# Kernel optimization log

Measured on AMD Instinct MI355X. Metric: run time of the kernel, lower is better.

## Reference

```python
import jax, jax.numpy as jnp
import numpy as np

DIM = 256
NUM_HEADS = 8
WH, WW = 7, 7
N = WH * WW
HEAD_DIM = DIM // NUM_HEADS
SCALE = HEAD_DIM ** -0.5
B_ = 4096
NW = 64  # windows per image


def _relative_position_index():
    # Swin relative position index: (N, N) int32 in [0, (2Wh-1)*(2Ww-1))
    coords = np.stack(np.meshgrid(np.arange(WH), np.arange(WW), indexing='ij'))  # (2, Wh, Ww)
    cf = coords.reshape(2, -1)  # (2, N)
    rel = cf[:, :, None] - cf[:, None, :]  # (2, N, N)
    rel = rel.transpose(1, 2, 0).copy()
    rel[:, :, 0] += WH - 1
    rel[:, :, 1] += WW - 1
    rel[:, :, 0] *= 2 * WW - 1
    return jnp.asarray(rel.sum(-1), dtype=jnp.int32)  # (N, N)


def setup_inputs() -> dict:
    key = jax.random.key(0)
    ks = jax.random.split(key, 7)
    x = jax.random.normal(ks[0], (B_, N, DIM), dtype=jnp.float32)
    mask = jax.random.normal(ks[1], (NW, N, N), dtype=jnp.float32)
    qkv_w = jax.random.normal(ks[2], (3 * DIM, DIM), dtype=jnp.float32) * 0.02
    qkv_b = jnp.zeros((3 * DIM,), dtype=jnp.float32)
    proj_w = jax.random.normal(ks[3], (DIM, DIM), dtype=jnp.float32) * 0.02
    proj_b = jnp.zeros((DIM,), dtype=jnp.float32)
    bias_table = jax.random.normal(ks[4], ((2 * WH - 1) * (2 * WW - 1), NUM_HEADS), dtype=jnp.float32) * 0.02
    rel_index = _relative_position_index()
    return {"x": x, "mask": mask, "qkv_w": qkv_w, "qkv_b": qkv_b,
            "proj_w": proj_w, "proj_b": proj_b, "bias_table": bias_table,
            "rel_index": rel_index}


def reference(x, mask, qkv_w, qkv_b, proj_w, proj_b, bias_table, rel_index):
    Bw, n, c = x.shape
    # qkv projection: (B_, N, 3C) -> (3, B_, nH, N, hd)
    qkv = (x @ qkv_w.T + qkv_b).reshape(Bw, n, 3, NUM_HEADS, HEAD_DIM)
    qkv = qkv.transpose(2, 0, 3, 1, 4)
    q, k, v = qkv[0], qkv[1], qkv[2]
    attn = jnp.einsum('bhqd,bhkd->bhqk', q * SCALE, k)  # (B_, nH, N, N)
    # gathered relative position bias: (nH, N, N)
    rpb = bias_table[rel_index.reshape(-1)].reshape(n, n, NUM_HEADS).transpose(2, 0, 1)
    attn = attn + rpb[None]
    # window mask: reshape batch into (B, nW) and broadcast mask per-window
    nW = mask.shape[0]
    attn = attn.reshape(Bw // nW, nW, NUM_HEADS, n, n) + mask[None, :, None]
    attn = attn.reshape(Bw, NUM_HEADS, n, n)
    attn = jax.nn.softmax(attn, axis=-1)
    out = jnp.einsum('bhqk,bhkd->bhqd', attn, v)  # (B_, nH, N, hd)
    out = out.transpose(0, 2, 1, 3).reshape(Bw, n, c)
    return out @ proj_w.T + proj_b
```

## Files before the change

### kernel.cpp

```cpp
#include <hip/hip_runtime.h>
#include <hip/hip_bf16.h>

typedef __bf16 bf16;
typedef __bf16 bf16x8 __attribute__((ext_vector_type(8)));
typedef float  f32x4  __attribute__((ext_vector_type(4)));

#define MFMA16(A,B,C) __builtin_amdgcn_mfma_f32_16x16x32_bf16((A),(B),(C),0,0,0)

constexpr float SCALE = 0.17677669529663687f;

constexpr size_t CB_OFF    = 0;
constexpr size_t QKVW_OFF  = 8388608;
constexpr size_t PROJW_OFF = QKVW_OFF + 768*256*2;
constexpr size_t QI_OFF    = PROJW_OFF + 256*256*2;
constexpr size_t TEN_ELEMS = 51380224ull;
constexpr size_t AO_OFF    = QI_OFF + 3*TEN_ELEMS*2;

__global__ __launch_bounds__(256) void build_cb_kernel(
    const float* __restrict__ bias_table, const float* __restrict__ mask,
    const int* __restrict__ rel_index, float* __restrict__ cb) {
  int idx = blockIdx.x * 256 + threadIdx.x;
  int j = idx & 63, m = (idx >> 6) & 63, h = (idx >> 12) & 7, w = idx >> 15;
  float v = 0.f;
  if (j < 49 && m < 49)
    v = bias_table[rel_index[m * 49 + j] * 8 + h] + mask[(w * 49 + m) * 49 + j];
  cb[idx] = v;
}

__global__ __launch_bounds__(256) void cvt_w_kernel(
    const float* __restrict__ qkv_w, const float* __restrict__ proj_w,
    bf16* __restrict__ qkv_wb, bf16* __restrict__ proj_wb) {
  int i = blockIdx.x * 256 + threadIdx.x;
  if (i < 768 * 256) qkv_wb[i] = (bf16)qkv_w[i];
  else               proj_wb[i - 768 * 256] = (bf16)proj_w[i - 768 * 256];
}

__device__ __forceinline__ bf16x8 frag(const bf16* S, int row, int kchunk) {
  return *reinterpret_cast<const bf16x8*>(&S[row * 64 + ((kchunk ^ (row & 7)) * 8)]);
}

__global__ __launch_bounds__(512, 2) void gemm_qkv_kernel(
    const float* __restrict__ x, const bf16* __restrict__ qkv_wb,
    const float* __restrict__ qkv_b, bf16* __restrict__ qkv_i) {
  __shared__ __align__(16) bf16 As[128 * 64];
  __shared__ __align__(16) bf16 Bs[256 * 64];
  const int bid = blockIdx.x;
  const int xcd = bid & 7, idx = bid >> 3;
  const int m_t = xcd * 196 + idx / 3;
  const int n_t = idx % 3;
  const int tid = threadIdx.x;
  const int wv = tid >> 6, l = tid & 63, l15 = l & 15, lgp = l >> 4;
  const int wr = wv >> 2, wc = wv & 3;

  const f32x4 fzero = {0.f, 0.f, 0.f, 0.f};
  f32x4 acc[4][4];
#pragma unroll
  for (int mt = 0; mt < 4; ++mt)
#pragma unroll
    for (int nt = 0; nt < 4; ++nt) acc[mt][nt] = fzero;

  for (int ks = 0; ks < 4; ++ks) {
    const int k0 = ks * 64;
#pragma unroll
    for (int i = 0; i < 2; ++i) {
      int c = i * 512 + tid;
      int row = c >> 3, kc = c & 7;
      const float* src = x + (size_t)(m_t * 128 + row) * 256 + k0 + kc * 8;
      f32x4 f0 = *reinterpret_cast<const f32x4*>(src);
      f32x4 f1 = *reinterpret_cast<const f32x4*>(src + 4);
      bf16x8 v8;
#pragma unroll
      for (int e = 0; e < 4; ++e) { v8[e] = (bf16)f0[e]; v8[e + 4] = (bf16)f1[e]; }
      *reinterpret_cast<bf16x8*>(&As[row * 64 + ((kc ^ (row & 7)) * 8)]) = v8;
    }
#pragma unroll
    for (int i = 0; i < 4; ++i) {
      int c = i * 512 + tid;
      int row = c >> 3, kc = c & 7;
      bf16x8 w8 = *reinterpret_cast<const bf16x8*>(
          qkv_wb + (size_t)(n_t * 256 + row) * 256 + k0 + kc * 8);
      *reinterpret_cast<bf16x8*>(&Bs[row * 64 + ((kc ^ (row & 7)) * 8)]) = w8;
    }
    __syncthreads();
#pragma unroll
    for (int kk = 0; kk < 2; ++kk) {
      bf16x8 Af[4], Bf[4];
#pragma unroll
      for (int mt = 0; mt < 4; ++mt) Af[mt] = frag(As, wr * 64 + mt * 16 + l15, kk * 4 + lgp);
#pragma unroll
      for (int nt = 0; nt < 4; ++nt) Bf[nt] = frag(Bs, wc * 64 + nt * 16 + l15, kk * 4 + lgp);
#pragma unroll
      for (int mt = 0; mt < 4; ++mt)
#pragma unroll
        for (int nt = 0; nt < 4; ++nt) acc[mt][nt] = MFMA16(Af[mt], Bf[nt], acc[mt][nt]);
    }
    __syncthreads();
  }

  bf16* tb = qkv_i + (size_t)n_t * TEN_ELEMS;
  const float sc = (n_t == 0) ? SCALE : 1.0f;
  float bias[4]; int hh[4], dd[4];
#pragma unroll
  for (int nt = 0; nt < 4; ++nt) {
    int n_g = n_t * 256 + wc * 64 + nt * 16 + l15;
    bias[nt] = qkv_b[n_g];
    int nl = n_g & 255;
    hh[nt] = nl >> 5; dd[nt] = nl & 31;
  }
#pragma unroll
  for (int mt = 0; mt < 4; ++mt) {
#pragma unroll
    for (int r = 0; r < 4; ++r) {
      int r_g = m_t * 128 + wr * 64 + mt * 16 + lgp * 4 + r;
      int b = r_g / 49, m = r_g - b * 49;
#pragma unroll
      for (int nt = 0; nt < 4; ++nt) {
        tb[((size_t)(b * 8 + hh[nt]) * 49 + m) * 32 + dd[nt]] =
            (bf16)((acc[mt][nt][r] + bias[nt]) * sc);
      }
    }
  }
}

__device__ __forceinline__ bf16x8 repack8(f32x4 Ta, f32x4 Tb, int l15, int lgp) {
  const int s0 = l15 + ((lgp & 1) << 5);
  const bool hi = (lgp & 2) != 0;
  bf16x8 F;
#pragma unroll
  for (int r = 0; r < 4; ++r) {
    float a0 = __shfl(Ta[r], s0);
    float b0 = __shfl(Tb[r], s0);
    F[r] = (bf16)(hi ? b0 : a0);
    float a1 = __shfl(Ta[r], s0 + 16);
    float b1 = __shfl(Tb[r], s0 + 16);
    F[r + 4] = (bf16)(hi ? b1 : a1);
  }
  return F;
}

__global__ __launch_bounds__(256) void attn_kernel(
    const bf16* __restrict__ qkv_i, const float* __restrict__ cb,
    bf16* __restrict__ ao) {
  __shared__ __align__(16) bf16 Vs[4][64 * 32];
  const int tid = threadIdx.x, wv = tid >> 6, l = tid & 63;
  const int l15 = l & 15, lgp = l >> 4;
  const int g = blockIdx.x * 4 + wv;
  const int b = g >> 3, h = g & 7;

  const bf16* qp = qkv_i + (size_t)(b * 8 + h) * 1568;
  const bf16* kp = qp + TEN_ELEMS;
  const bf16* vp = kp + TEN_ELEMS;
  bf16* vsm = &Vs[wv][0];

#pragma unroll
  for (int i = 0; i < 4; ++i) {
    int c = i * 64 + l;
    if (c < 196)
      *reinterpret_cast<bf16x8*>(&vsm[c * 8]) =
          *reinterpret_cast<const bf16x8*>(vp + c * 8);
  }
  {
    const bf16x8 z8 = {(bf16)0.f,(bf16)0.f,(bf16)0.f,(bf16)0.f,
                       (bf16)0.f,(bf16)0.f,(bf16)0.f,(bf16)0.f};
    if (l < 60) *reinterpret_cast<bf16x8*>(&vsm[1568 + l * 8]) = z8;
  }
  __syncthreads();

  bf16x8 Qf[4], Kf[4];
#pragma unroll
  for (int mt = 0; mt < 4; ++mt) {
    int m = mt * 16 + l15; int mc = m < 49 ? m : 48;
    Qf[mt] = *reinterpret_cast<const bf16x8*>(qp + mc * 32 + lgp * 8);
  }
#pragma unroll
  for (int jt = 0; jt < 4; ++jt) {
    int j = jt * 16 + l15; int jc = j < 49 ? j : 48;
    Kf[jt] = *reinterpret_cast<const bf16x8*>(kp + jc * 32 + lgp * 8);
  }
  bf16x8 Vb[2][2];
#pragma unroll
  for (int dt = 0; dt < 2; ++dt)
#pragma unroll
    for (int ksx = 0; ksx < 2; ++ksx) {
#pragma unroll
      for (int u = 0; u < 8; ++u) {
        int j = ksx * 32 + lgp * 8 + u;
        Vb[dt][ksx][u] = vsm[j * 32 + dt * 16 + l15];
      }
    }

  const float* cbp = cb + (size_t)((b & 63) * 8 + h) * 4096;
  bf16* aob = ao + (size_t)b * 12544;
  const f32x4 fzero = {0.f, 0.f, 0.f, 0.f};

#pragma unroll
  for (int mt = 0; mt < 4; ++mt) {
    int mrow = mt * 16 + l15;
    f32x4 e4[4];
#pragma unroll
    for (int jt = 0; jt < 4; ++jt) e4[jt] = MFMA16(Kf[jt], Qf[mt], fzero);
#pragma unroll
    for (int jt = 0; jt < 4; ++jt) {
      f32x4 c4 = *reinterpret_cast<const f32x4*>(cbp + mrow * 64 + jt * 16 + lgp * 4);
#pragma unroll
      for (int r = 0; r < 4; ++r) e4[jt][r] += c4[r];
    }
    if (lgp != 0) { e4[3][0] = -3.0e38f; }
    e4[3][1] = -3.0e38f; e4[3][2] = -3.0e38f; e4[3][3] = -3.0e38f;

    float mx = e4[0][0];
#pragma unroll
    for (int jt = 0; jt < 4; ++jt)
#pragma unroll
      for (int r = 0; r < 4; ++r) mx = fmaxf(mx, e4[jt][r]);
    mx = fmaxf(mx, __shfl_xor(mx, 16));
    mx = fmaxf(mx, __shfl_xor(mx, 32));
    float sum = 0.f;
#pragma unroll
    for (int jt = 0; jt < 4; ++jt)
#pragma unroll
      for (int r = 0; r < 4; ++r) {
        float ex = __expf(e4[jt][r] - mx);
        e4[jt][r] = ex;
        sum += ex;
      }
    sum += __shfl_xor(sum, 16);
    sum += __shfl_xor(sum, 32);
    float rinv = 1.0f / sum;
#pragma unroll
    for (int jt = 0; jt < 4; ++jt)
#pragma unroll
      for (int r = 0; r < 4; ++r) e4[jt][r] *= rinv;

    bf16x8 Pf0 = repack8(e4[0], e4[1], l15, lgp);
    bf16x8 Pf1 = repack8(e4[2], e4[3], l15, lgp);
    f32x4 pv[2];
#pragma unroll
    for (int dt = 0; dt < 2; ++dt) {
      pv[dt] = MFMA16(Pf0, Vb[dt][0], fzero);
      pv[dt] = MFMA16(Pf1, Vb[dt][1], pv[dt]);
    }
#pragma unroll
    for (int r = 0; r < 4; ++r) {
      int m_g = mt * 16 + lgp * 4 + r;
      if (m_g < 49) {
#pragma unroll
        for (int dt = 0; dt < 2; ++dt)
          aob[m_g * 256 + h * 32 + dt * 16 + l15] = (bf16)pv[dt][r];
      }
    }
  }
}

__global__ __launch_bounds__(512, 2) void gemm_proj_kernel(
    const bf16* __restrict__ ao, const bf16* __restrict__ proj_wb,
    const float* __restrict__ proj_b, float* __restrict__ out) {
  __shared__ __align__(16) bf16 As[128 * 64];
  __shared__ __align__(16) bf16 Bs[256 * 64];
  const int bid = blockIdx.x;
  const int xcd = bid & 7, idx = bid >> 3;
  const int m_t = xcd * 196 + idx;
  const int tid = threadIdx.x;
  const int wv = tid >> 6, l = tid & 63, l15 = l & 15, lgp = l >> 4;
  const int wr = wv >> 2, wc = wv & 3;

  const f32x4 fzero = {0.f, 0.f, 0.f, 0.f};
  f32x4 acc[4][4];
#pragma unroll
  for (int mt = 0; mt < 4; ++mt)
#pragma unroll
    for (int nt = 0; nt < 4; ++nt) acc[mt][nt] = fzero;

  for (int ks = 0; ks < 4; ++ks) {
    const int k0 = ks * 64;
#pragma unroll
    for (int i = 0; i < 2; ++i) {
      int c = i * 512 + tid;
      int row = c >> 3, kc = c & 7;
      bf16x8 a8 = *reinterpret_cast<const bf16x8*>(
          ao + (size_t)(m_t * 128 + row) * 256 + k0 + kc * 8);
      *reinterpret_cast<bf16x8*>(&As[row * 64 + ((kc ^ (row & 7)) * 8)]) = a8;
    }
#pragma unroll
    for (int i = 0; i < 4; ++i) {
      int c = i * 512 + tid;
      int row = c >> 3, kc = c & 7;
      bf16x8 w8 = *reinterpret_cast<const bf16x8*>(
          proj_wb + (size_t)row * 256 + k0 + kc * 8);
      *reinterpret_cast<bf16x8*>(&Bs[row * 64 + ((kc ^ (row & 7)) * 8)]) = w8;
    }
    __syncthreads();
#pragma unroll
    for (int kk = 0; kk < 2; ++kk) {
      bf16x8 Af[4], Bf[4];
#pragma unroll
      for (int mt = 0; mt < 4; ++mt) Af[mt] = frag(As, wr * 64 + mt * 16 + l15, kk * 4 + lgp);
#pragma unroll
      for (int nt = 0; nt < 4; ++nt) Bf[nt] = frag(Bs, wc * 64 + nt * 16 + l15, kk * 4 + lgp);
#pragma unroll
      for (int mt = 0; mt < 4; ++mt)
#pragma unroll
        for (int nt = 0; nt < 4; ++nt) acc[mt][nt] = MFMA16(Af[mt], Bf[nt], acc[mt][nt]);
    }
    __syncthreads();
  }

  float bias[4]; int cg[4];
#pragma unroll
  for (int nt = 0; nt < 4; ++nt) {
    cg[nt] = wc * 64 + nt * 16 + l15;
    bias[nt] = proj_b[cg[nt]];
  }
#pragma unroll
  for (int mt = 0; mt < 4; ++mt) {
#pragma unroll
    for (int r = 0; r < 4; ++r) {
      size_t r_g = (size_t)(m_t * 128 + wr * 64 + mt * 16 + lgp * 4 + r);
#pragma unroll
      for (int nt = 0; nt < 4; ++nt)
        out[r_g * 256 + cg[nt]] = acc[mt][nt][r] + bias[nt];
    }
  }
}

extern "C" void kernel_launch(void* const* d_in, const int* in_sizes, int n_in,
                              void* d_out, int out_size, void* d_ws, size_t ws_size,
                              hipStream_t stream) {
  const float* x          = (const float*)d_in[0];
  const float* mask       = (const float*)d_in[1];
  const float* qkv_w      = (const float*)d_in[2];
  const float* qkv_b      = (const float*)d_in[3];
  const float* proj_w     = (const float*)d_in[4];
  const float* proj_b     = (const float*)d_in[5];
  const float* bias_table = (const float*)d_in[6];
  const int*   rel_index  = (const int*)d_in[7];

  char* ws = (char*)d_ws;
  float* cb      = (float*)(ws + CB_OFF);
  bf16*  qkv_wb  = (bf16*)(ws + QKVW_OFF);
  bf16*  proj_wb = (bf16*)(ws + PROJW_OFF);
  bf16*  qkv_i   = (bf16*)(ws + QI_OFF);
  bf16*  ao      = (bf16*)(ws + AO_OFF);

  hipLaunchKernelGGL(build_cb_kernel, dim3(8192), dim3(256), 0, stream,
                     bias_table, mask, rel_index, cb);
  hipLaunchKernelGGL(cvt_w_kernel, dim3(1024), dim3(256), 0, stream,
                     qkv_w, proj_w, qkv_wb, proj_wb);
  hipLaunchKernelGGL(gemm_qkv_kernel, dim3(4704), dim3(512), 0, stream,
                     x, qkv_wb, qkv_b, qkv_i);
  hipLaunchKernelGGL(attn_kernel, dim3(8192), dim3(256), 0, stream,
                     qkv_i, cb, ao);
  hipLaunchKernelGGL(gemm_proj_kernel, dim3(1568), dim3(512), 0, stream,
                     ao, proj_wb, proj_b, (float*)d_out);
}
```

Baseline: 453.1 us.

## Rewrite QKV GEMM as register-resident weight panels streaming x without LDS

```diff
diff --git a/kernel.cpp b/kernel.cpp
--- a/kernel.cpp
+++ b/kernel.cpp
@@ -39,84 +39,68 @@
   return *reinterpret_cast<const bf16x8*>(&S[row * 64 + ((kchunk ^ (row & 7)) * 8)]);
 }
 
-__global__ __launch_bounds__(512, 2) void gemm_qkv_kernel(
+__global__ __launch_bounds__(256, 2) void gemm_qkv_kernel(
     const float* __restrict__ x, const bf16* __restrict__ qkv_wb,
     const float* __restrict__ qkv_b, bf16* __restrict__ qkv_i) {
-  __shared__ __align__(16) bf16 As[128 * 64];
-  __shared__ __align__(16) bf16 Bs[256 * 64];
-  const int bid = blockIdx.x;
-  const int xcd = bid & 7, idx = bid >> 3;
-  const int m_t = xcd * 196 + idx / 3;
-  const int n_t = idx % 3;
+  const int bid    = blockIdx.x;
+  const int panel  = bid / 1568;
+  const int mchunk = bid - panel * 1568;
+  const int xcd    = mchunk & 7, mc = mchunk >> 3;
+  const int m_base = (xcd * 196 + mc) * 128;
   const int tid = threadIdx.x;
   const int wv = tid >> 6, l = tid & 63, l15 = l & 15, lgp = l >> 4;
-  const int wr = wv >> 2, wc = wv & 3;
 
   const f32x4 fzero = {0.f, 0.f, 0.f, 0.f};
-  f32x4 acc[4][4];
-#pragma unroll
-  for (int mt = 0; mt < 4; ++mt)
-#pragma unroll
-    for (int nt = 0; nt < 4; ++nt) acc[mt][nt] = fzero;
-
-  for (int ks = 0; ks < 4; ++ks) {
-    const int k0 = ks * 64;
-#pragma unroll
-    for (int i = 0; i < 2; ++i) {
-      int c = i * 512 + tid;
-      int row = c >> 3, kc = c & 7;
-      const float* src = x + (size_t)(m_t * 128 + row) * 256 + k0 + kc * 8;
-      f32x4 f0 = *reinterpret_cast<const f32x4*>(src);
-      f32x4 f1 = *reinterpret_cast<const f32x4*>(src + 4);
-      bf16x8 v8;
-#pragma unroll
-      for (int e = 0; e < 4; ++e) { v8[e] = (bf16)f0[e]; v8[e + 4] = (bf16)f1[e]; }
-      *reinterpret_cast<bf16x8*>(&As[row * 64 + ((kc ^ (row & 7)) * 8)]) = v8;
-    }
-#pragma unroll
-    for (int i = 0; i < 4; ++i) {
-      int c = i * 512 + tid;
-      int row = c >> 3, kc = c & 7;
-      bf16x8 w8 = *reinterpret_cast<const bf16x8*>(
-          qkv_wb + (size_t)(n_t * 256 + row) * 256 + k0 + kc * 8);
-      *reinterpret_cast<bf16x8*>(&Bs[row * 64 + ((kc ^ (row & 7)) * 8)]) = w8;
-    }
-    __syncthreads();
-#pragma unroll
-    for (int kk = 0; kk < 2; ++kk) {
-      bf16x8 Af[4], Bf[4];
-#pragma unroll
-      for (int mt = 0; mt < 4; ++mt) Af[mt] = frag(As, wr * 64 + mt * 16 + l15, kk * 4 + lgp);
-#pragma unroll
-      for (int nt = 0; nt < 4; ++nt) Bf[nt] = frag(Bs, wc * 64 + nt * 16 + l15, kk * 4 + lgp);
-#pragma unroll
-      for (int mt = 0; mt < 4; ++mt)
-#pragma unroll
-        for (int nt = 0; nt < 4; ++nt) acc[mt][nt] = MFMA16(Af[mt], Bf[nt], acc[mt][nt]);
-    }
-    __syncthreads();
-  }
-
-  bf16* tb = qkv_i + (size_t)n_t * TEN_ELEMS;
-  const float sc = (n_t == 0) ? SCALE : 1.0f;
-  float bias[4]; int hh[4], dd[4];
+  const int n0 = panel * 256 + wv * 64;
+
+  bf16x8 Bf[4][8];
+#pragma unroll
+  for (int nt = 0; nt < 4; ++nt)
+#pragma unroll
+    for (int ks = 0; ks < 8; ++ks)
+      Bf[nt][ks] = *reinterpret_cast<const bf16x8*>(
+          qkv_wb + (size_t)(n0 + nt * 16 + l15) * 256 + ks * 32 + lgp * 8);
+
+  float bias[4];
+  int   hh[4], ddb[4];
 #pragma unroll
   for (int nt = 0; nt < 4; ++nt) {
-    int n_g = n_t * 256 + wc * 64 + nt * 16 + l15;
-    bias[nt] = qkv_b[n_g];
-    int nl = n_g & 255;
-    hh[nt] = nl >> 5; dd[nt] = nl & 31;
-  }
-#pragma unroll
-  for (int mt = 0; mt < 4; ++mt) {
+    bias[nt] = qkv_b[n0 + nt * 16 + l15];
+    int n_l = wv * 64 + nt * 16;
+    hh[nt] = n_l >> 5; ddb[nt] = n_l & 31;
+  }
+  const float sc = (panel == 0) ? SCALE : 1.0f;
+  bf16* tb = qkv_i + (size_t)panel * TEN_ELEMS;
+
+  for (int sub = 0; sub < 8; ++sub) {
+    const int m0 = m_base + sub * 16;
+    const float* xrow = x + (size_t)(m0 + l15) * 256 + lgp * 8;
+    f32x4 a0[8], a1[8];
+#pragma unroll
+    for (int ks = 0; ks < 8; ++ks) {
+      a0[ks] = *reinterpret_cast<const f32x4*>(xrow + ks * 32);
+      a1[ks] = *reinterpret_cast<const f32x4*>(xrow + ks * 32 + 4);
+    }
+    f32x4 acc[4] = {fzero, fzero, fzero, fzero};
+#pragma unroll
+    for (int ks = 0; ks < 8; ++ks) {
+      bf16x8 Af;
+#pragma unroll
+      for (int e = 0; e < 4; ++e) {
+        Af[e]     = (bf16)a0[ks][e];
+        Af[e + 4] = (bf16)a1[ks][e];
+      }
+#pragma unroll
+      for (int nt = 0; nt < 4; ++nt) acc[nt] = MFMA16(Af, Bf[nt][ks], acc[nt]);
+    }
 #pragma unroll
     for (int r = 0; r < 4; ++r) {
-      int r_g = m_t * 128 + wr * 64 + mt * 16 + lgp * 4 + r;
-      int b = r_g / 49, m = r_g - b * 49;
+      int m_g = m0 + lgp * 4 + r;
+      int b = m_g / 49, m = m_g - b * 49;
 #pragma unroll
       for (int nt = 0; nt < 4; ++nt) {
-        tb[((size_t)(b * 8 + hh[nt]) * 49 + m) * 32 + dd[nt]] =
-            (bf16)((acc[mt][nt][r] + bias[nt]) * sc);
+        tb[((size_t)(b * 8 + hh[nt]) * 49 + m) * 32 + ddb[nt] + l15] =
+            (bf16)((acc[nt][r] + bias[nt]) * sc);
       }
     }
   }
@@ -346,7 +330,7 @@
                      bias_table, mask, rel_index, cb);
   hipLaunchKernelGGL(cvt_w_kernel, dim3(1024), dim3(256), 0, stream,
                      qkv_w, proj_w, qkv_wb, proj_wb);
-  hipLaunchKernelGGL(gemm_qkv_kernel, dim3(4704), dim3(512), 0, stream,
+  hipLaunchKernelGGL(gemm_qkv_kernel, dim3(4704), dim3(256), 0, stream,
                      x, qkv_wb, qkv_b, qkv_i);
   hipLaunchKernelGGL(attn_kernel, dim3(8192), dim3(256), 0, stream,
                      qkv_i, cb, ao);
```

After: 604.7 us. +33.5%, slower.
